# Performance work log

Hardware: AMD Instinct MI355X
Metric: run time of the kernel (lower is better)

The kernel has to match this reference:

```python
import jax, jax.numpy as jnp
import numpy as np

N = 100000
E = 3200000
NEG_SLOPE = 0.2  # PyG GATConv default


def gat_layer(x, src, dst, W, a_src, a_dst, b, heads, out_ch, concat):
    # per-node linear transform, split into heads: [N, H, C]
    h = (x @ W).reshape(N, heads, out_ch)
    # per-node attention logits: [N, H]
    al_src = jnp.sum(h * a_src, axis=-1)
    al_dst = jnp.sum(h * a_dst, axis=-1)
    # per-edge attention coefficient (x_j = source, x_i = target): [E, H]
    e = jax.nn.leaky_relu(al_src[src] + al_dst[dst], NEG_SLOPE)
    # segment softmax over incoming edges of each destination node
    m = jax.ops.segment_max(e, dst, num_segments=N)
    e = jnp.exp(e - m[dst])
    denom = jax.ops.segment_sum(e, dst, num_segments=N)
    alpha = e / (denom[dst] + 1e-16)
    # weighted message aggregation: scatter-add over dst
    msg = h[src] * alpha[..., None]  # [E, H, C]
    out = jax.ops.segment_sum(msg, dst, num_segments=N)  # [N, H, C]
    out = out.reshape(N, heads * out_ch) if concat else out.mean(axis=1)
    return out + b


def setup_inputs() -> dict:
    key = jax.random.key(0)
    ks = jax.random.split(key, 11)
    return {
        "x": jax.random.normal(ks[0], (N, 2), dtype=jnp.float32),
        "edge_index": jax.random.randint(ks[1], (2, E), 0, N, dtype=jnp.int64),
        "edge_attr": jax.random.normal(ks[2], (E, 1), dtype=jnp.float32),
        "W1": jax.random.normal(ks[3], (2, 32), dtype=jnp.float32) * 0.5,
        "att_src1": jax.random.normal(ks[4], (4, 8), dtype=jnp.float32) * 0.3,
        "att_dst1": jax.random.normal(ks[5], (4, 8), dtype=jnp.float32) * 0.3,
        "b1": jnp.zeros((32,), dtype=jnp.float32),
        "W2": jax.random.normal(ks[6], (32, 2), dtype=jnp.float32) * 0.2,
        "att_src2": jax.random.normal(ks[7], (1, 2), dtype=jnp.float32) * 0.3,
        "att_dst2": jax.random.normal(ks[8], (1, 2), dtype=jnp.float32) * 0.3,
        "b2": jnp.zeros((2,), dtype=jnp.float32),
    }


def reference(x, edge_index, edge_attr, W1, att_src1, att_dst1, b1, W2, att_src2, att_dst2, b2):
    # add self-loops (PyG GATConv default add_self_loops=True)
    loops = jnp.arange(N, dtype=edge_index.dtype)
    src = jnp.concatenate([edge_index[0], loops])
    dst = jnp.concatenate([edge_index[1], loops])
    h = gat_layer(x, src, dst, W1, att_src1, att_dst1, b1, heads=4, out_ch=8, concat=True)
    h = jax.nn.elu(h)
    out = gat_layer(h, src, dst, W2, att_src2, att_dst2, b2, heads=1, out_ch=2, concat=False)
    return out
```

## Files before the change

### kernel.cpp

```cpp
#include <hip/hip_runtime.h>
#include <math.h>

#define NEG_SLOPE 0.2f
#define BK_BITS 8
#define BK (1 << BK_BITS)
#define SBITS 17
#define SMASK ((1 << SBITS) - 1)
#define CAP 9216
#define PPT1 9
#define SW(p) ((p) ^ (((p) >> 5) & 31))
#define BCUR(b) ((b) * 16)

__device__ __forceinline__ float lrelu(float x) { return x > 0.f ? x : NEG_SLOPE * x; }

__global__ __launch_bounds__(1024) void bucket_scatter(const int* __restrict__ src,
                                                       const int* __restrict__ dst,
                                                       int* __restrict__ bcur,
                                                       int* __restrict__ pairs, int E) {
    __shared__ int cnt[512], off[512], cur[512], adj[512];
    __shared__ int2 lpair[12504];
    __shared__ int sTot;
    int t = threadIdx.x;
    int blk = blockIdx.x;
    int nb = gridDim.x;
    if (t < 512) cnt[t] = 0;
    __syncthreads();

    int E4 = E >> 2;
    int chunk4 = (E4 + nb - 1) / nb;
    const int4* src4 = (const int4*)src;
    const int4* dst4 = (const int4*)dst;
    int base4 = blk * chunk4;
    int4 d4[4], s4[4];
    bool val[4];
#pragma unroll
    for (int k = 0; k < 4; k++) {
        int o = k * 1024 + t;
        int i4 = base4 + o;
        val[k] = (o < chunk4) && (i4 < E4);
        if (val[k]) { d4[k] = dst4[i4]; s4[k] = src4[i4]; }
    }
    int dt = -1, st = 0;
    if (blk == nb - 1) {
        int e = (E4 << 2) + t;
        if (e < E) { dt = dst[e]; st = src[e]; }
    }
#pragma unroll
    for (int k = 0; k < 4; k++) {
        if (val[k]) {
            atomicAdd(&cnt[d4[k].x >> BK_BITS], 1);
            atomicAdd(&cnt[d4[k].y >> BK_BITS], 1);
            atomicAdd(&cnt[d4[k].z >> BK_BITS], 1);
            atomicAdd(&cnt[d4[k].w >> BK_BITS], 1);
        }
    }
    if (dt >= 0) atomicAdd(&cnt[dt >> BK_BITS], 1);
    __syncthreads();

    if (t < 64) {
        int v[8], mysum = 0;
#pragma unroll
        for (int k = 0; k < 8; k++) { v[k] = cnt[t * 8 + k]; mysum += v[k]; }
        int s = mysum;
#pragma unroll
        for (int o = 1; o < 64; o <<= 1) {
            int u = __shfl_up(s, o);
            if (t >= o) s += u;
        }
        int run = s - mysum;
#pragma unroll
        for (int k = 0; k < 8; k++) {
            int d2 = t * 8 + k;
            off[d2] = run; cur[d2] = run;
            run += v[k];
        }
        if (t == 63) sTot = s;
    }
    __syncthreads();
    if (t < 512 && cnt[t] > 0) {
        int g0 = atomicAdd(&bcur[BCUR(t)], cnt[t]);
        adj[t] = t * CAP + g0 - off[t];
    }
    __syncthreads();
    int total = sTot;

#pragma unroll
    for (int k = 0; k < 4; k++) {
        if (val[k]) {
            int slot;
            slot = atomicAdd(&cur[d4[k].x >> BK_BITS], 1); lpair[slot] = make_int2(d4[k].x, s4[k].x);
            slot = atomicAdd(&cur[d4[k].y >> BK_BITS], 1); lpair[slot] = make_int2(d4[k].y, s4[k].y);
            slot = atomicAdd(&cur[d4[k].z >> BK_BITS], 1); lpair[slot] = make_int2(d4[k].z, s4[k].z);
            slot = atomicAdd(&cur[d4[k].w >> BK_BITS], 1); lpair[slot] = make_int2(d4[k].w, s4[k].w);
        }
    }
    if (dt >= 0) {
        int slot = atomicAdd(&cur[dt >> BK_BITS], 1);
        lpair[slot] = make_int2(dt, st);
    }
    __syncthreads();

    for (int i = t; i < total; i += 1024) {
        int2 e = lpair[i];
        int b = e.x >> BK_BITS;
        int pos = adj[b] + i;
        if (pos - b * CAP < CAP)
            pairs[pos] = ((e.x & (BK - 1)) << SBITS) | e.y;
    }
}

__global__ __launch_bounds__(1024) void agg1_sortgather(
        const int* __restrict__ pairs, const int* __restrict__ bcur,
        const float2* __restrict__ x2,
        const float* __restrict__ W1, const float* __restrict__ asrc,
        const float* __restrict__ adst, const float* __restrict__ b1,
        const float* __restrict__ W2, const float* __restrict__ as2,
        const float* __restrict__ ad2,
        float2* __restrict__ h2, float* __restrict__ al2d,
        int* __restrict__ rowdeg, int* __restrict__ pairs2, int N) {
    __shared__ float sW[64], sB[32], sW2[64], sP[4], sQ[4], sPd[4], sQd[4], sA2[4];
    __shared__ int cnt[BK], off[BK], cur[BK];
    __shared__ int sorted[CAP];
    int t = threadIdx.x;
    int b = blockIdx.x;
    if (t < 64) { sW[t] = W1[t]; sW2[t] = W2[t]; }
    if (t < 32) sB[t] = b1[t];
    if (t < 2) { sA2[t] = as2[t]; sA2[2 + t] = ad2[t]; }
    if (t >= 64 && t < 68) {
        int tt = t - 64;
        float P = 0.f, Q = 0.f, Pd = 0.f, Qd = 0.f;
#pragma unroll
        for (int k = 0; k < 8; k++) {
            int c = tt * 8 + k;
            float a = asrc[c], ad_ = adst[c];
            float w0 = W1[c], w1 = W1[32 + c];
            P += w0 * a; Q += w1 * a;
            Pd += w0 * ad_; Qd += w1 * ad_;
        }
        sP[tt] = P; sQ[tt] = Q; sPd[tt] = Pd; sQd[tt] = Qd;
    }
    if (t >= 512 && t < 512 + BK) cnt[t - 512] = 0;
    __syncthreads();

    int dbase = b << BK_BITS;
    int ndst = min(BK, N - dbase);
    int lo = b * CAP;
    int hi = lo + min(bcur[BCUR(b)], CAP);

    int myp[PPT1];
#pragma unroll
    for (int k = 0; k < PPT1; k++) {
        int i = lo + t + k * 1024;
        myp[k] = (i < hi) ? pairs[i] : -1;
    }
#pragma unroll
    for (int k = 0; k < PPT1; k++) {
        if (myp[k] >= 0) atomicAdd(&cnt[myp[k] >> SBITS], 1);
    }
    __syncthreads();

    if (t < 64) {
        int v[4], mysum = 0;
#pragma unroll
        for (int k = 0; k < 4; k++) { v[k] = cnt[t * 4 + k]; mysum += v[k]; }
        int s = mysum;
#pragma unroll
        for (int o = 1; o < 64; o <<= 1) {
            int u = __shfl_up(s, o);
            if (t >= o) s += u;
        }
        int run = s - mysum;
#pragma unroll
        for (int k = 0; k < 4; k++) {
            int d2 = t * 4 + k;
            off[d2] = run; cur[d2] = run;
            run += v[k];
        }
    }
    __syncthreads();

#pragma unroll
    for (int k = 0; k < PPT1; k++) {
        int p = myp[k];
        if (p >= 0) {
            int pos = atomicAdd(&cur[p >> SBITS], 1);
            sorted[SW(pos)] = p & SMASK;
        }
    }
    __syncthreads();

    for (int i = t; i < CAP; i += 1024) pairs2[b * CAP + i] = sorted[SW(i)];
    if (t < ndst) rowdeg[dbase + t] = (off[t] << 8) | min(cnt[t], 255);

    int d = t >> 2, q = t & 3;
    if (d < ndst) {
        int n = dbase + d;
        float rP[4], rQ[4], ald[4];
        float2 xd = x2[n];
#pragma unroll
        for (int h = 0; h < 4; h++) {
            rP[h] = sP[h]; rQ[h] = sQ[h];
            ald[h] = xd.x * sPd[h] + xd.y * sQd[h];
        }
        int deg = cnt[d];
        int start = off[d];
        int ids[16];
#pragma unroll
        for (int k = 0; k < 16; k++) {
            int j = q + 4 * k;
            ids[k] = (j < deg) ? sorted[SW(start + j)] : -1;
        }
        float Sw[4] = {0.f, 0.f, 0.f, 0.f};
        float S0[4] = {0.f, 0.f, 0.f, 0.f};
        float S1[4] = {0.f, 0.f, 0.f, 0.f};
#pragma unroll
        for (int half = 0; half < 2; half++) {
            float2 xv[8];
#pragma unroll
            for (int k = 0; k < 8; k++) {
                int id = ids[half * 8 + k];
                xv[k] = x2[id >= 0 ? id : 0];
            }
#pragma unroll
            for (int k = 0; k < 8; k++) {
                if (ids[half * 8 + k] >= 0) {
#pragma unroll
                    for (int h = 0; h < 4; h++) {
                        float e = lrelu(fmaf(xv[k].x, rP[h], fmaf(xv[k].y, rQ[h], ald[h])));
                        float w = __expf(fminf(e, 80.f));
                        Sw[h] += w; S0[h] += w * xv[k].x; S1[h] += w * xv[k].y;
                    }
                }
            }
        }
        for (int j = q + 64; j < deg; j += 4) {
            int s = sorted[SW(start + j)];
            float2 xs = x2[s];
#pragma unroll
            for (int h = 0; h < 4; h++) {
                float e = lrelu(fmaf(xs.x, rP[h], fmaf(xs.y, rQ[h], ald[h])));
                float w = __expf(fminf(e, 80.f));
                Sw[h] += w; S0[h] += w * xs.x; S1[h] += w * xs.y;
            }
        }
#pragma unroll
        for (int o = 1; o <= 2; o <<= 1) {
#pragma unroll
            for (int h = 0; h < 4; h++) {
                Sw[h] += __shfl_xor(Sw[h], o);
                S0[h] += __shfl_xor(S0[h], o);
                S1[h] += __shfl_xor(S1[h], o);
            }
        }
#pragma unroll
        for (int h = 0; h < 4; h++) {
            float e = lrelu(fmaf(xd.x, rP[h], fmaf(xd.y, rQ[h], ald[h])));
            float w = __expf(fminf(e, 80.f));
            Sw[h] += w; S0[h] += w * xd.x; S1[h] += w * xd.y;
        }
        float rq = 1.f / (Sw[q] + 1e-16f);
        float s0q = S0[q], s1q = S1[q];
        float h20 = 0.f, h21 = 0.f;
#pragma unroll
        for (int k = 0; k < 8; k++) {
            int c = q * 8 + k;
            float outc = (sW[c] * s0q + sW[32 + c] * s1q) * rq;
            float v2 = outc + sB[c];
            v2 = v2 > 0.f ? v2 : __expf(v2) - 1.f;
            h20 = fmaf(v2, sW2[2 * c], h20);
            h21 = fmaf(v2, sW2[2 * c + 1], h21);
        }
#pragma unroll
        for (int o = 1; o <= 2; o <<= 1) {
            h20 += __shfl_xor(h20, o);
            h21 += __shfl_xor(h21, o);
        }
        if (q == 0) {
            h2[n] = make_float2(h20, h21);
            al2d[n] = h20 * sA2[2] + h21 * sA2[3];
        }
    }
}

__global__ __launch_bounds__(1024) void agg2_gather(
        const int* __restrict__ pairs2, const int* __restrict__ rowdeg,
        const float2* __restrict__ h2, const float* __restrict__ al2d,
        const float* __restrict__ as2, const float* __restrict__ b2,
        float2* __restrict__ out, int N) {
    int t = threadIdx.x;
    int b = blockIdx.x;
    int dbase = b << BK_BITS;
    int ndst = min(BK, N - dbase);
    int d = t >> 2, q = t & 3;
    if (d >= ndst) return;
    float a0 = as2[0], a1 = as2[1];

    int n = dbase + d;
    int rd = rowdeg[n];
    int start = rd >> 8;
    int deg = rd & 255;
    const int* lst = pairs2 + b * CAP + start;
    float ald = al2d[n];
    float2 hd = h2[n];
    int ids[16];
#pragma unroll
    for (int k = 0; k < 16; k++) {
        int j = q + 4 * k;
        ids[k] = (j < deg) ? lst[j] : -1;
    }
    float wsum = 0.f, ax = 0.f, ay = 0.f;
#pragma unroll
    for (int half = 0; half < 2; half++) {
        float2 hv[8];
#pragma unroll
        for (int k = 0; k < 8; k++) {
            int id = ids[half * 8 + k];
            hv[k] = h2[id >= 0 ? id : 0];
        }
#pragma unroll
        for (int k = 0; k < 8; k++) {
            if (ids[half * 8 + k] >= 0) {
                float e = lrelu(fmaf(hv[k].x, a0, fmaf(hv[k].y, a1, ald)));
                float w = __expf(fminf(e, 80.f));
                wsum += w; ax = fmaf(w, hv[k].x, ax); ay = fmaf(w, hv[k].y, ay);
            }
        }
    }
    for (int j = q + 64; j < deg; j += 4) {
        int s = lst[j];
        float2 hv = h2[s];
        float e = lrelu(fmaf(hv.x, a0, fmaf(hv.y, a1, ald)));
        float w = __expf(fminf(e, 80.f));
        wsum += w; ax = fmaf(w, hv.x, ax); ay = fmaf(w, hv.y, ay);
    }
#pragma unroll
    for (int o = 1; o <= 2; o <<= 1) {
        wsum += __shfl_xor(wsum, o);
        ax += __shfl_xor(ax, o);
        ay += __shfl_xor(ay, o);
    }
    if (q == 0) {
        float e = lrelu(fmaf(hd.x, a0, fmaf(hd.y, a1, ald)));
        float w = __expf(fminf(e, 80.f));
        wsum += w; ax = fmaf(w, hd.x, ax); ay = fmaf(w, hd.y, ay);
        float inv = 1.f / (wsum + 1e-16f);
        out[n] = make_float2(ax * inv + b2[0], ay * inv + b2[1]);
    }
}

extern "C" void kernel_launch(void* const* d_in, const int* in_sizes, int n_in,
                              void* d_out, int out_size, void* d_ws, size_t ws_size,
                              hipStream_t stream) {
    const float* x     = (const float*)d_in[0];
    const int*   eidx  = (const int*)d_in[1];
    const float* W1    = (const float*)d_in[3];
    const float* asrc1 = (const float*)d_in[4];
    const float* adst1 = (const float*)d_in[5];
    const float* b1    = (const float*)d_in[6];
    const float* W2    = (const float*)d_in[7];
    const float* asrc2 = (const float*)d_in[8];
    const float* adst2 = (const float*)d_in[9];
    const float* b2    = (const float*)d_in[10];

    const int N = in_sizes[0] / 2;
    const int E = in_sizes[1] / 2;
    const int* src = eidx;
    const int* dst = eidx + E;
    const int NB = (N + BK - 1) >> BK_BITS;
    const int nblk = 256;

    float* w = (float*)d_ws;
    float2* h2    = (float2*)w;
    float*  al2d  = w + 2 * (size_t)N;
    int* ip       = (int*)(w + 3 * (size_t)N);
    int* rowdeg   = ip;
    int* bcur     = ip + (size_t)N;
    int* pairs    = bcur + 8192;
    int* pairs2   = pairs + (size_t)NB * CAP;

    hipMemsetAsync(bcur, 0, 8192 * sizeof(int), stream);
    bucket_scatter<<<nblk, 1024, 0, stream>>>(src, dst, bcur, pairs, E);
    agg1_sortgather<<<NB, 1024, 0, stream>>>(pairs, bcur, (const float2*)x,
                                             W1, asrc1, adst1, b1, W2, asrc2, adst2,
                                             h2, al2d, rowdeg, pairs2, N);
    agg2_gather<<<NB, 1024, 0, stream>>>(pairs2, rowdeg, (const float2*)h2, al2d,
                                         asrc2, b2, (float2*)d_out, N);
}
```

Baseline: 157.0 us.

## Partition destinations into 256 buckets of 391 nodes via magic division

Replaces power-of-two destination buckets (256 nodes each, ~391 buckets) with exactly 256 buckets of 391 nodes, computed by multiply-shift division. Every kernel now launches 256 blocks, matching the CU count, and the aggregation kernels loop over two chunks of destinations per block. Bucket capacity and per-thread pair counts grow to match, and the scan widens to 448 entries. This aims to remove the tail wave and load imbalance of having more blocks than CUs, at the cost of more shared memory and registers per block and a serial second pass inside each block.

```diff
diff --git a/kernel.cpp b/kernel.cpp
--- a/kernel.cpp
+++ b/kernel.cpp
@@ -2,28 +2,31 @@
 #include <math.h>
 
 #define NEG_SLOPE 0.2f
-#define BK_BITS 8
-#define BK (1 << BK_BITS)
+#define NBK 256
+#define DPB 391
+#define MAGIC 10984572ULL
 #define SBITS 17
 #define SMASK ((1 << SBITS) - 1)
-#define CAP 9216
-#define PPT1 9
+#define CAP 14336
+#define PPT1 14
+#define SCN 448
 #define SW(p) ((p) ^ (((p) >> 5) & 31))
 #define BCUR(b) ((b) * 16)
 
 __device__ __forceinline__ float lrelu(float x) { return x > 0.f ? x : NEG_SLOPE * x; }
+__device__ __forceinline__ int bkt(int d) { return (int)(((unsigned long long)(unsigned)d * MAGIC) >> 32); }
 
 __global__ __launch_bounds__(1024) void bucket_scatter(const int* __restrict__ src,
                                                        const int* __restrict__ dst,
                                                        int* __restrict__ bcur,
                                                        int* __restrict__ pairs, int E) {
-    __shared__ int cnt[512], off[512], cur[512], adj[512];
+    __shared__ int cnt[NBK], off[NBK], cur[NBK], adj[NBK];
     __shared__ int2 lpair[12504];
     __shared__ int sTot;
     int t = threadIdx.x;
     int blk = blockIdx.x;
     int nb = gridDim.x;
-    if (t < 512) cnt[t] = 0;
+    if (t < NBK) cnt[t] = 0;
     __syncthreads();
 
     int E4 = E >> 2;
@@ -48,19 +51,19 @@
 #pragma unroll
     for (int k = 0; k < 4; k++) {
         if (val[k]) {
-            atomicAdd(&cnt[d4[k].x >> BK_BITS], 1);
-            atomicAdd(&cnt[d4[k].y >> BK_BITS], 1);
-            atomicAdd(&cnt[d4[k].z >> BK_BITS], 1);
-            atomicAdd(&cnt[d4[k].w >> BK_BITS], 1);
-        }
-    }
-    if (dt >= 0) atomicAdd(&cnt[dt >> BK_BITS], 1);
+            atomicAdd(&cnt[bkt(d4[k].x)], 1);
+            atomicAdd(&cnt[bkt(d4[k].y)], 1);
+            atomicAdd(&cnt[bkt(d4[k].z)], 1);
+            atomicAdd(&cnt[bkt(d4[k].w)], 1);
+        }
+    }
+    if (dt >= 0) atomicAdd(&cnt[bkt(dt)], 1);
     __syncthreads();
 
     if (t < 64) {
-        int v[8], mysum = 0;
-#pragma unroll
-        for (int k = 0; k < 8; k++) { v[k] = cnt[t * 8 + k]; mysum += v[k]; }
+        int v[4], mysum = 0;
+#pragma unroll
+        for (int k = 0; k < 4; k++) { v[k] = cnt[t * 4 + k]; mysum += v[k]; }
         int s = mysum;
 #pragma unroll
         for (int o = 1; o < 64; o <<= 1) {
@@ -69,15 +72,15 @@
         }
         int run = s - mysum;
 #pragma unroll
-        for (int k = 0; k < 8; k++) {
-            int d2 = t * 8 + k;
+        for (int k = 0; k < 4; k++) {
+            int d2 = t * 4 + k;
             off[d2] = run; cur[d2] = run;
             run += v[k];
         }
         if (t == 63) sTot = s;
     }
     __syncthreads();
-    if (t < 512 && cnt[t] > 0) {
+    if (t < NBK && cnt[t] > 0) {
         int g0 = atomicAdd(&bcur[BCUR(t)], cnt[t]);
         adj[t] = t * CAP + g0 - off[t];
     }
@@ -88,24 +91,24 @@
     for (int k = 0; k < 4; k++) {
         if (val[k]) {
             int slot;
-            slot = atomicAdd(&cur[d4[k].x >> BK_BITS], 1); lpair[slot] = make_int2(d4[k].x, s4[k].x);
-            slot = atomicAdd(&cur[d4[k].y >> BK_BITS], 1); lpair[slot] = make_int2(d4[k].y, s4[k].y);
-            slot = atomicAdd(&cur[d4[k].z >> BK_BITS], 1); lpair[slot] = make_int2(d4[k].z, s4[k].z);
-            slot = atomicAdd(&cur[d4[k].w >> BK_BITS], 1); lpair[slot] = make_int2(d4[k].w, s4[k].w);
+            slot = atomicAdd(&cur[bkt(d4[k].x)], 1); lpair[slot] = make_int2(d4[k].x, s4[k].x);
+            slot = atomicAdd(&cur[bkt(d4[k].y)], 1); lpair[slot] = make_int2(d4[k].y, s4[k].y);
+            slot = atomicAdd(&cur[bkt(d4[k].z)], 1); lpair[slot] = make_int2(d4[k].z, s4[k].z);
+            slot = atomicAdd(&cur[bkt(d4[k].w)], 1); lpair[slot] = make_int2(d4[k].w, s4[k].w);
         }
     }
     if (dt >= 0) {
-        int slot = atomicAdd(&cur[dt >> BK_BITS], 1);
+        int slot = atomicAdd(&cur[bkt(dt)], 1);
         lpair[slot] = make_int2(dt, st);
     }
     __syncthreads();
 
     for (int i = t; i < total; i += 1024) {
         int2 e = lpair[i];
-        int b = e.x >> BK_BITS;
+        int b = bkt(e.x);
         int pos = adj[b] + i;
         if (pos - b * CAP < CAP)
-            pairs[pos] = ((e.x & (BK - 1)) << SBITS) | e.y;
+            pairs[pos] = ((e.x - b * DPB) << SBITS) | e.y;
     }
 }
 
@@ -119,7 +122,7 @@
         float2* __restrict__ h2, float* __restrict__ al2d,
         int* __restrict__ rowdeg, int* __restrict__ pairs2, int N) {
     __shared__ float sW[64], sB[32], sW2[64], sP[4], sQ[4], sPd[4], sQd[4], sA2[4];
-    __shared__ int cnt[BK], off[BK], cur[BK];
+    __shared__ int cnt[SCN], off[SCN], cur[SCN];
     __shared__ int sorted[CAP];
     int t = threadIdx.x;
     int b = blockIdx.x;
@@ -139,11 +142,11 @@
         }
         sP[tt] = P; sQ[tt] = Q; sPd[tt] = Pd; sQd[tt] = Qd;
     }
-    if (t >= 512 && t < 512 + BK) cnt[t - 512] = 0;
-    __syncthreads();
-
-    int dbase = b << BK_BITS;
-    int ndst = min(BK, N - dbase);
+    if (t >= 512 && t < 512 + SCN) cnt[t - 512] = 0;
+    __syncthreads();
+
+    int dbase = b * DPB;
+    int ndst = min(DPB, N - dbase);
     int lo = b * CAP;
     int hi = lo + min(bcur[BCUR(b)], CAP);
 
@@ -160,9 +163,9 @@
     __syncthreads();
 
     if (t < 64) {
-        int v[4], mysum = 0;
-#pragma unroll
-        for (int k = 0; k < 4; k++) { v[k] = cnt[t * 4 + k]; mysum += v[k]; }
+        int v[7], mysum = 0;
+#pragma unroll
+        for (int k = 0; k < 7; k++) { v[k] = cnt[t * 7 + k]; mysum += v[k]; }
         int s = mysum;
 #pragma unroll
         for (int o = 1; o < 64; o <<= 1) {
@@ -171,8 +174,8 @@
         }
         int run = s - mysum;
 #pragma unroll
-        for (int k = 0; k < 4; k++) {
-            int d2 = t * 4 + k;
+        for (int k = 0; k < 7; k++) {
+            int d2 = t * 7 + k;
             off[d2] = run; cur[d2] = run;
             run += v[k];
         }
@@ -192,8 +195,10 @@
     for (int i = t; i < CAP; i += 1024) pairs2[b * CAP + i] = sorted[SW(i)];
     if (t < ndst) rowdeg[dbase + t] = (off[t] << 8) | min(cnt[t], 255);
 
-    int d = t >> 2, q = t & 3;
-    if (d < ndst) {
+    int q = t & 3;
+    for (int ch = 0; ch < 2; ch++) {
+        int d = ch * 256 + (t >> 2);
+        if (d >= ndst) break;
         int n = dbase + d;
         float rP[4], rQ[4], ald[4];
         float2 xd = x2[n];
@@ -289,62 +294,65 @@
         float2* __restrict__ out, int N) {
     int t = threadIdx.x;
     int b = blockIdx.x;
-    int dbase = b << BK_BITS;
-    int ndst = min(BK, N - dbase);
-    int d = t >> 2, q = t & 3;
-    if (d >= ndst) return;
+    int dbase = b * DPB;
+    int ndst = min(DPB, N - dbase);
+    int q = t & 3;
     float a0 = as2[0], a1 = as2[1];
 
-    int n = dbase + d;
-    int rd = rowdeg[n];
-    int start = rd >> 8;
-    int deg = rd & 255;
-    const int* lst = pairs2 + b * CAP + start;
-    float ald = al2d[n];
-    float2 hd = h2[n];
-    int ids[16];
-#pragma unroll
-    for (int k = 0; k < 16; k++) {
-        int j = q + 4 * k;
-        ids[k] = (j < deg) ? lst[j] : -1;
-    }
-    float wsum = 0.f, ax = 0.f, ay = 0.f;
-#pragma unroll
-    for (int half = 0; half < 2; half++) {
-        float2 hv[8];
-#pragma unroll
-        for (int k = 0; k < 8; k++) {
-            int id = ids[half * 8 + k];
-            hv[k] = h2[id >= 0 ? id : 0];
-        }
-#pragma unroll
-        for (int k = 0; k < 8; k++) {
-            if (ids[half * 8 + k] >= 0) {
-                float e = lrelu(fmaf(hv[k].x, a0, fmaf(hv[k].y, a1, ald)));
-                float w = __expf(fminf(e, 80.f));
-                wsum += w; ax = fmaf(w, hv[k].x, ax); ay = fmaf(w, hv[k].y, ay);
-            }
-        }
-    }
-    for (int j = q + 64; j < deg; j += 4) {
-        int s = lst[j];
-        float2 hv = h2[s];
-        float e = lrelu(fmaf(hv.x, a0, fmaf(hv.y, a1, ald)));
-        float w = __expf(fminf(e, 80.f));
-        wsum += w; ax = fmaf(w, hv.x, ax); ay = fmaf(w, hv.y, ay);
-    }
-#pragma unroll
-    for (int o = 1; o <= 2; o <<= 1) {
-        wsum += __shfl_xor(wsum, o);
-        ax += __shfl_xor(ax, o);
-        ay += __shfl_xor(ay, o);
-    }
-    if (q == 0) {
-        float e = lrelu(fmaf(hd.x, a0, fmaf(hd.y, a1, ald)));
-        float w = __expf(fminf(e, 80.f));
-        wsum += w; ax = fmaf(w, hd.x, ax); ay = fmaf(w, hd.y, ay);
-        float inv = 1.f / (wsum + 1e-16f);
-        out[n] = make_float2(ax * inv + b2[0], ay * inv + b2[1]);
+    for (int ch = 0; ch < 2; ch++) {
+        int d = ch * 256 + (t >> 2);
+        if (d >= ndst) break;
+        int n = dbase + d;
+        int rd = rowdeg[n];
+        int start = rd >> 8;
+        int deg = rd & 255;
+        const int* lst = pairs2 + b * CAP + start;
+        float ald = al2d[n];
+        float2 hd = h2[n];
+        int ids[16];
+#pragma unroll
+        for (int k = 0; k < 16; k++) {
+            int j = q + 4 * k;
+            ids[k] = (j < deg) ? lst[j] : -1;
+        }
+        float wsum = 0.f, ax = 0.f, ay = 0.f;
+#pragma unroll
+        for (int half = 0; half < 2; half++) {
+            float2 hv[8];
+#pragma unroll
+            for (int k = 0; k < 8; k++) {
+                int id = ids[half * 8 + k];
+                hv[k] = h2[id >= 0 ? id : 0];
+            }
+#pragma unroll
+            for (int k = 0; k < 8; k++) {
+                if (ids[half * 8 + k] >= 0) {
+                    float e = lrelu(fmaf(hv[k].x, a0, fmaf(hv[k].y, a1, ald)));
+                    float w = __expf(fminf(e, 80.f));
+                    wsum += w; ax = fmaf(w, hv[k].x, ax); ay = fmaf(w, hv[k].y, ay);
+                }
+            }
+        }
+        for (int j = q + 64; j < deg; j += 4) {
+            int s = lst[j];
+            float2 hv = h2[s];
+            float e = lrelu(fmaf(hv.x, a0, fmaf(hv.y, a1, ald)));
+            float w = __expf(fminf(e, 80.f));
+            wsum += w; ax = fmaf(w, hv.x, ax); ay = fmaf(w, hv.y, ay);
+        }
+#pragma unroll
+        for (int o = 1; o <= 2; o <<= 1) {
+            wsum += __shfl_xor(wsum, o);
+            ax += __shfl_xor(ax, o);
+            ay += __shfl_xor(ay, o);
+        }
+        if (q == 0) {
+            float e = lrelu(fmaf(hd.x, a0, fmaf(hd.y, a1, ald)));
+            float w = __expf(fminf(e, 80.f));
+            wsum += w; ax = fmaf(w, hd.x, ax); ay = fmaf(w, hd.y, ay);
+            float inv = 1.f / (wsum + 1e-16f);
+            out[n] = make_float2(ax * inv + b2[0], ay * inv + b2[1]);
+        }
     }
 }
 
@@ -366,8 +374,6 @@
     const int E = in_sizes[1] / 2;
     const int* src = eidx;
     const int* dst = eidx + E;
-    const int NB = (N + BK - 1) >> BK_BITS;
-    const int nblk = 256;
 
     float* w = (float*)d_ws;
     float2* h2    = (float2*)w;
@@ -375,14 +381,14 @@
     int* ip       = (int*)(w + 3 * (size_t)N);
     int* rowdeg   = ip;
     int* bcur     = ip + (size_t)N;
-    int* pairs    = bcur + 8192;
-    int* pairs2   = pairs + (size_t)NB * CAP;
-
-    hipMemsetAsync(bcur, 0, 8192 * sizeof(int), stream);
-    bucket_scatter<<<nblk, 1024, 0, stream>>>(src, dst, bcur, pairs, E);
-    agg1_sortgather<<<NB, 1024, 0, stream>>>(pairs, bcur, (const float2*)x,
-                                             W1, asrc1, adst1, b1, W2, asrc2, adst2,
-                                             h2, al2d, rowdeg, pairs2, N);
-    agg2_gather<<<NB, 1024, 0, stream>>>(pairs2, rowdeg, (const float2*)h2, al2d,
-                                         asrc2, b2, (float2*)d_out, N);
+    int* pairs    = bcur + 4096;
+    int* pairs2   = pairs + (size_t)NBK * CAP;
+
+    hipMemsetAsync(bcur, 0, 4096 * sizeof(int), stream);
+    bucket_scatter<<<NBK, 1024, 0, stream>>>(src, dst, bcur, pairs, E);
+    agg1_sortgather<<<NBK, 1024, 0, stream>>>(pairs, bcur, (const float2*)x,
+                                              W1, asrc1, adst1, b1, W2, asrc2, adst2,
+                                              h2, al2d, rowdeg, pairs2, N);
+    agg2_gather<<<NBK, 1024, 0, stream>>>(pairs2, rowdeg, (const float2*)h2, al2d,
+                                          asrc2, b2, (float2*)d_out, N);
 }
```

After: 151.4 us. 3.6% less time.
